# Kernel optimization log

Hardware: AMD Instinct MI355X
Metric: run time of the kernel (lower is better)

## Reference

```python
import jax, jax.numpy as jnp
import numpy as np

N, E, G = 2048, 4096, 128      # nodes, edges, graphs
H, IN, ED = 128, 11, 4         # hidden, input node feat, edge feat
BN_EPS = 1e-5


def setup_inputs() -> dict:
    key = jax.random.key(0)
    ks = iter(jax.random.split(key, 40))
    r = lambda shape, s=0.1: jax.random.normal(next(ks), shape, jnp.float32) * s
    inp = dict(
        x=r((N, IN), 1.0),
        edge_attr=jax.random.uniform(next(ks), (E, ED), jnp.float32),
        edge_index=jax.random.randint(next(ks), (2, E), 0, N).astype(jnp.int32),
        batch=jnp.sort(jax.random.randint(next(ks), (N,), 0, G)).astype(jnp.int32),
        # layer 0 (in=11 -> out=128)
        w1_0=r((ED, H)), b1_0=jnp.zeros(H), w2_0=r((H, IN * H), 0.02), b2_0=jnp.zeros(IN * H),
        root_0=r((IN, H)), bias_0=jnp.zeros(H),
        bn_g0=jnp.ones(H), bn_b0=jnp.zeros(H), bn_m0=r((H,), 0.1),
        bn_v0=jax.random.uniform(next(ks), (H,), jnp.float32, 0.5, 1.5),
        # layers 1..4 stacked (in=out=128)
        w1_s=r((4, ED, H)), b1_s=jnp.zeros((4, H)), w2_s=r((4, H, H * H), 0.02), b2_s=jnp.zeros((4, H * H)),
        root_s=r((4, H, H)), bias_s=jnp.zeros((4, H)),
        bn_gs=jnp.ones((4, H)), bn_bs=jnp.zeros((4, H)), bn_ms=r((4, H), 0.1),
        bn_vs=jax.random.uniform(next(ks), (4, H), jnp.float32, 0.5, 1.5),
        # readout MLP
        lin1_w=r((H, H // 2)), lin1_b=jnp.zeros(H // 2),
        lin2_w=r((H // 2, 1)), lin2_b=jnp.zeros(1),
    )
    return inp


def _nnconv(x, src, dst, edge_attr, w1, b1, w2, b2, root, bias):
    in_c = x.shape[-1]
    h = jax.nn.relu(edge_attr @ w1 + b1)                 # [E, H]
    w_e = (h @ w2 + b2).reshape(-1, in_c, H)             # [E, in, H] per-edge weight
    msg = jnp.einsum('ei,eio->eo', x[src], w_e)          # gather + per-edge matvec
    s = jax.ops.segment_sum(msg, dst, num_segments=N)
    cnt = jax.ops.segment_sum(jnp.ones(dst.shape, x.dtype), dst, num_segments=N)
    aggr = s / jnp.maximum(cnt, 1.0)[:, None]            # scatter-mean
    return aggr + x @ root + bias


def _bn_eval(x, g, b, m, v):
    return (x - m) * jax.lax.rsqrt(v + BN_EPS) * g + b


def reference(x, edge_attr, w1_0, b1_0, w2_0, b2_0, root_0, bias_0,
              bn_g0, bn_b0, bn_m0, bn_v0,
              w1_s, b1_s, w2_s, b2_s, root_s, bias_s,
              bn_gs, bn_bs, bn_ms, bn_vs,
              lin1_w, lin1_b, lin2_w, lin2_b,
              edge_index, batch):
    src, dst = edge_index[0], edge_index[1]
    # layer 0
    h = jax.nn.relu(_bn_eval(
        _nnconv(x, src, dst, edge_attr, w1_0, b1_0, w2_0, b2_0, root_0, bias_0),
        bn_g0, bn_b0, bn_m0, bn_v0))
    # layers 1..4 with residual (dims match)
    for l in range(4):
        h_new = jax.nn.relu(_bn_eval(
            _nnconv(h, src, dst, edge_attr, w1_s[l], b1_s[l], w2_s[l], b2_s[l], root_s[l], bias_s[l]),
            bn_gs[l], bn_bs[l], bn_ms[l], bn_vs[l]))
        h = h + h_new
    # global mean pool over graphs
    gs = jax.ops.segment_sum(h, batch, num_segments=G)
    gc = jax.ops.segment_sum(jnp.ones((N,), h.dtype), batch, num_segments=G)
    g = gs / jnp.maximum(gc, 1.0)[:, None]
    # readout (dropout is identity in eval mode)
    g = jax.nn.relu(g @ lin1_w + lin1_b)
    return g @ lin2_w + lin2_b
```

## Files before the change

### kernel.cpp

```cpp
#include <hip/hip_runtime.h>
#include <cstdint>
#include <cstddef>

#define NN 2048
#define NE 4096
#define NG 128
#define HD 128
#define SKM 16
#define SK0 5
#define NCH 64
#define CHE 64

typedef __attribute__((ext_vector_type(8))) _Float16 f16x8;
typedef __attribute__((ext_vector_type(4))) float f32x4;

#define GLOAD_LDS16(gptr, lptr)                                                          \
  __builtin_amdgcn_global_load_lds((const __attribute__((address_space(1))) unsigned int*)(gptr), \
                                   (__attribute__((address_space(3))) unsigned int*)(lptr), 16, 0, 0)

__global__ __launch_bounds__(256) void k_prep(
    const float* __restrict__ ea,
    const float* __restrict__ w1_0, const float* __restrict__ b1_0,
    const float* __restrict__ w1_s, const float* __restrict__ b1_s,
    const float* __restrict__ x,
    const float* __restrict__ w2_0, const float* __restrict__ b2_0,
    const float* __restrict__ w2s, const float* __restrict__ b2s,
    const int* __restrict__ dst, int* __restrict__ hist,
    _Float16* __restrict__ hb, _Float16* __restrict__ x16,
    _Float16* __restrict__ w2T0, _Float16* __restrict__ w2T) {
  __shared__ float sld[64][65];
  const int bid = blockIdx.x, t = threadIdx.x;

  if (bid < 10240) {
    int idx = bid * 256 + t;
    int c = idx & (HD - 1);
    int e = (idx >> 7) & (NE - 1);
    int l = idx >> 19;
    const float* w1 = (l == 0) ? w1_0 : (w1_s + (size_t)(l - 1) * 4 * HD);
    const float* b1 = (l == 0) ? b1_0 : (b1_s + (size_t)(l - 1) * HD);
    float4 a = *(const float4*)(ea + (size_t)e * 4);
    float v = b1[c] + a.x * w1[c] + a.y * w1[HD + c] + a.z * w1[2 * HD + c] + a.w * w1[3 * HD + c];
    hb[idx] = (_Float16)fmaxf(v, 0.f);
  } else if (bid < 10368) {
    int idx = (bid - 10240) * 256 + t;
    int n = idx >> 4, i = idx & 15;
    x16[idx] = (_Float16)(i < 11 ? x[(size_t)n * 11 + i] : 0.f);
  } else if (bid < 10496) {
    int o = bid - 10368;
    for (int kap = t; kap < 2080; kap += 256) {
      int k = kap >> 4, i = kap & 15;
      float v = 0.f;
      if (i < 11) {
        if (k < 128) v = w2_0[(size_t)k * 1408 + i * 128 + o];
        else if (k == 128) v = b2_0[i * 128 + o];
      }
      w2T0[(size_t)o * 2080 + kap] = (_Float16)v;
    }
  } else if (bid < 12560) {
    int idx2 = bid - 10496;
    int l = idx2 / 516;
    int rem = idx2 - l * 516;
    int ob = rem / 258;
    int kb = rem - ob * 258;
    const float* w2 = w2s + (size_t)l * 16384 * 128;
    const float* b2 = b2s + (size_t)l * 128 * 128;
    _Float16* outp = w2T + (size_t)l * 128 * 16512;
    int k0 = kb * 64, o0 = ob * 64;
    int r = t >> 4, c4 = (t & 15) * 4;
#pragma unroll
    for (int it = 0; it < 4; ++it) {
      int kk = k0 + r + it * 16;
      const float* srcp = (kk < 16384) ? (w2 + (size_t)kk * 128 + o0 + c4)
                                       : (b2 + (size_t)(kk - 16384) * 128 + o0 + c4);
      *(float4*)&sld[r + it * 16][c4] = *(const float4*)srcp;
    }
    __syncthreads();
    int rr = t >> 3, c8 = (t & 7) * 8;
#pragma unroll
    for (int it = 0; it < 2; ++it) {
      int ol = rr + it * 32;
      _Float16 pk[8];
#pragma unroll
      for (int j = 0; j < 8; ++j) pk[j] = (_Float16)sld[c8 + j][ol];
      *(f16x8*)(outp + (size_t)(o0 + ol) * 16512 + k0 + c8) = *(const f16x8*)pk;
    }
  } else {
    int e = (bid - 12560) * 256 + t;
    if (e < NE) atomicAdd(&hist[(e >> 6) * NN + dst[e]], 1);
  }
}

__global__ __launch_bounds__(1024) void k_scan2(const int* __restrict__ hist,
                                                int* __restrict__ rowptr,
                                                int* __restrict__ chunkoff,
                                                const int* __restrict__ batch,
                                                int* __restrict__ gstart) {
  __shared__ int s[NN];
  int t = threadIdx.x;
  int c0 = 0, c1 = 0;
  for (int c = 0; c < NCH; ++c) { c0 += hist[c * NN + t]; c1 += hist[c * NN + t + 1024]; }
  s[t] = c0; s[t + 1024] = c1;
  __syncthreads();
  for (int d = 1; d < NN; d <<= 1) {
    int a0 = s[t], a1 = s[t + 1024];
    int v0 = (t >= d) ? s[t - d] : 0;
    int v1 = (t + 1024 >= d) ? s[t + 1024 - d] : 0;
    __syncthreads();
    s[t] = a0 + v0; s[t + 1024] = a1 + v1;
    __syncthreads();
  }
  rowptr[t + 1] = s[t]; rowptr[t + 1025] = s[t + 1024];
  if (t == 0) rowptr[0] = 0;
  int run0 = s[t] - c0, run1 = s[t + 1024] - c1;
  for (int c = 0; c < NCH; ++c) {
    chunkoff[c * NN + t] = run0;        run0 += hist[c * NN + t];
    chunkoff[c * NN + t + 1024] = run1; run1 += hist[c * NN + t + 1024];
  }
  if (t <= NG) {
    int lo = 0, hi = NN;
    while (lo < hi) { int mid = (lo + hi) >> 1; if (batch[mid] < t) lo = mid + 1; else hi = mid; }
    gstart[t] = lo;
  }
}

__global__ __launch_bounds__(64) void k_fill2(const int* __restrict__ dst,
                                              const int* __restrict__ chunkoff,
                                              int* __restrict__ elist) {
  __shared__ int sd[CHE];
  int c = blockIdx.x, t = threadIdx.x;
  int e = c * CHE + t;
  int dv = dst[e];
  sd[t] = dv;
  __syncthreads();
  int lrank = 0;
  for (int j = 0; j < t; ++j) lrank += (sd[j] == dv) ? 1 : 0;
  elist[chunkoff[c * NN + dv] + lrank] = e;
}

__global__ __launch_bounds__(256, 2) void k_mma0(
    const _Float16* __restrict__ xh,
    const _Float16* __restrict__ hb,
    const _Float16* __restrict__ w2T,
    const int* __restrict__ src,
    _Float16* __restrict__ msgp) {
  constexpr int KT = 2080;
  __shared__ _Float16 Bs[2][4096];
  __shared__ _Float16 hTl[26][128];

  const int tid = threadIdx.x;
  const int e0 = blockIdx.x * 128;
  const int w = tid >> 6, l = tid & 63, l16 = l & 15, g = l >> 4;

  const int k0 = blockIdx.y * 13, nk = 13;
  const int kb = k0 * 2;

  int nd[8];
#pragma unroll
  for (int mt = 0; mt < 8; ++mt) nd[mt] = src[e0 + mt * 16 + l16];

  for (int idx = tid; idx < 26 * 128; idx += 256) {
    int kk = idx >> 7, m = idx & 127;
    int k = kb + kk;
    _Float16 v;
    if (k < 128) v = hb[(size_t)(e0 + m) * 128 + k];
    else v = (k == 128) ? (_Float16)1.0f : (_Float16)0.0f;
    hTl[kk][m] = v;
  }

  f16x8 xr[8];
#pragma unroll
  for (int mt = 0; mt < 8; ++mt)
    xr[mt] = *(const f16x8*)(xh + (size_t)nd[mt] * 16 + (g & 1) * 8);

  auto stageB = [&](int buf, int c) {
    const int kap0 = c * 32;
#pragma unroll
    for (int j2 = 0; j2 < 2; ++j2) {
      int ntg = w * 2 + j2;
      const _Float16* gp = w2T + (size_t)(ntg * 16 + l16) * KT + kap0 + g * 8;
      GLOAD_LDS16(gp, &Bs[buf][(w * 128 + j2 * 64) * 8]);
    }
  };

  stageB(0, k0);
  __syncthreads();

  f32x4 acc[8][2];
#pragma unroll
  for (int mt = 0; mt < 8; ++mt)
#pragma unroll
    for (int jj = 0; jj < 2; ++jj) acc[mt][jj] = (f32x4){0.f, 0.f, 0.f, 0.f};

  int buf = 0;
  for (int j = 0; j < nk; ++j) {
    if (j + 1 < nk) {
      stageB(buf ^ 1, k0 + j + 1);
      asm volatile("s_waitcnt vmcnt(2)" ::: "memory");
    } else {
      asm volatile("s_waitcnt vmcnt(0)" ::: "memory");
    }
    __builtin_amdgcn_sched_barrier(0);

    f16x8 bv0 = *(const f16x8*)&Bs[buf][(size_t)(w * 2 + 0) * 512 + l * 8];
    f16x8 bv1 = *(const f16x8*)&Bs[buf][(size_t)(w * 2 + 1) * 512 + l * 8];
#pragma unroll
    for (int mt = 0; mt < 8; ++mt) {
      _Float16 hh = hTl[2 * j + (g >> 1)][mt * 16 + l16];
      f16x8 hv = {hh, hh, hh, hh, hh, hh, hh, hh};
      f16x8 av = xr[mt] * hv;
      acc[mt][0] = __builtin_amdgcn_mfma_f32_16x16x32_f16(av, bv0, acc[mt][0], 0, 0, 0);
      acc[mt][1] = __builtin_amdgcn_mfma_f32_16x16x32_f16(av, bv1, acc[mt][1], 0, 0, 0);
    }
    buf ^= 1;
    __syncthreads();
  }

  _Float16* mp = msgp + ((size_t)blockIdx.y * NE + e0) * 128;
#pragma unroll
  for (int mt = 0; mt < 8; ++mt)
#pragma unroll
    for (int jj = 0; jj < 2; ++jj)
#pragma unroll
      for (int r = 0; r < 4; ++r) {
        int row = mt * 16 + 4 * g + r;
        mp[(size_t)row * 128 + w * 32 + jj * 16 + l16] = (_Float16)acc[mt][jj][r];
      }
}

__global__ __launch_bounds__(256, 2) void k_mma4(
    const _Float16* __restrict__ xh,
    const _Float16* __restrict__ hb,
    const _Float16* __restrict__ w2T,
    const int* __restrict__ src,
    _Float16* __restrict__ msgp) {
  constexpr int KT = 16512;
  __shared__ __align__(16) _Float16 Bs[2][4096];

  const int tid = threadIdx.x;
  const int w = tid >> 6, l = tid & 63, l16 = l & 15, g = l >> 4;
  const int e0 = blockIdx.x * 128;
  const int sk = blockIdx.y;
  const int k0 = sk * 8;
  const bool haveBias = (sk == 15);

  int nd[8];
#pragma unroll
  for (int mt = 0; mt < 8; ++mt) nd[mt] = src[e0 + mt * 16 + l16];

  f16x8 hv[8];
#pragma unroll
  for (int mt = 0; mt < 8; ++mt)
    hv[mt] = *(const f16x8*)(hb + (size_t)(e0 + mt * 16 + l16) * 128 + k0);

  auto stageB = [&](int buf, int kap0) {
#pragma unroll
    for (int j2 = 0; j2 < 2; ++j2) {
      const _Float16* gp = w2T + (size_t)((w * 2 + j2) * 16 + l16) * KT + kap0 + g * 8;
      GLOAD_LDS16(gp, &Bs[buf][(w * 2 + j2) * 512]);
    }
  };

  f32x4 acc[8][2];
#pragma unroll
  for (int mt = 0; mt < 8; ++mt) {
    acc[mt][0] = (f32x4){0.f, 0.f, 0.f, 0.f};
    acc[mt][1] = (f32x4){0.f, 0.f, 0.f, 0.f};
  }

  int buf = 0;
  stageB(0, k0 * 128);

#define CONSUME(AV_EXPR)                                                              \
  {                                                                                   \
    f16x8 bv0 = *(const f16x8*)&Bs[buf][(w * 2 + 0) * 512 + l * 8];                   \
    f16x8 bv1 = *(const f16x8*)&Bs[buf][(w * 2 + 1) * 512 + l * 8];                   \
    _Pragma("unroll")                                                                 \
    for (int mt = 0; mt < 8; ++mt) {                                                  \
      f16x8 av = (AV_EXPR);                                                           \
      acc[mt][0] = __builtin_amdgcn_mfma_f32_16x16x32_f16(av, bv0, acc[mt][0], 0, 0, 0); \
      acc[mt][1] = __builtin_amdgcn_mfma_f32_16x16x32_f16(av, bv1, acc[mt][1], 0, 0, 0); \
    }                                                                                 \
    buf ^= 1;                                                                         \
  }

#pragma unroll
  for (int win = 0; win < 4; ++win) {
    f16x8 xw[8];
#pragma unroll
    for (int mt = 0; mt < 8; ++mt)
      xw[mt] = *(const f16x8*)(xh + (size_t)nd[mt] * 128 + win * 32 + g * 8);

#pragma unroll
    for (int jk = 0; jk < 8; ++jk) {
      if (jk < 7) {
        stageB(buf ^ 1, (k0 + jk + 1) * 128 + win * 32);
        asm volatile("s_waitcnt vmcnt(2)" ::: "memory");
      } else if (haveBias) {
        stageB(buf ^ 1, 16384 + win * 32);
        asm volatile("s_waitcnt vmcnt(2)" ::: "memory");
      } else if (win < 3) {
        stageB(buf ^ 1, k0 * 128 + (win + 1) * 32);
        asm volatile("s_waitcnt vmcnt(2)" ::: "memory");
      } else {
        asm volatile("s_waitcnt vmcnt(0)" ::: "memory");
      }
      __builtin_amdgcn_sched_barrier(0);
      _Float16 hh;
      CONSUME(({ hh = hv[mt][jk];
                 f16x8 hs = {hh, hh, hh, hh, hh, hh, hh, hh};
                 xw[mt] * hs; }));
    }
    if (haveBias) {
      if (win < 3) {
        stageB(buf ^ 1, k0 * 128 + (win + 1) * 32);
        asm volatile("s_waitcnt vmcnt(2)" ::: "memory");
      } else {
        asm volatile("s_waitcnt vmcnt(0)" ::: "memory");
      }
      __builtin_amdgcn_sched_barrier(0);
      CONSUME((xw[mt]));
    }
  }
#undef CONSUME

  _Float16* mp = msgp + ((size_t)sk * NE + e0) * 128;
#pragma unroll
  for (int mt = 0; mt < 8; ++mt)
#pragma unroll
    for (int jj = 0; jj < 2; ++jj)
#pragma unroll
      for (int r = 0; r < 4; ++r) {
        int row = mt * 16 + 4 * g + r;
        mp[(size_t)row * 128 + w * 32 + jj * 16 + l16] = (_Float16)acc[mt][jj][r];
      }
}

template <int NSK>
__global__ __launch_bounds__(256) void k_msum(const _Float16* __restrict__ msgp,
                                              float* __restrict__ msgf) {
  int idx = blockIdx.x * 256 + threadIdx.x;
  const _Float16* p = msgp + (size_t)idx * 8;
  float s0 = 0.f, s1 = 0.f, s2 = 0.f, s3 = 0.f, s4 = 0.f, s5 = 0.f, s6 = 0.f, s7 = 0.f;
#pragma unroll
  for (int k = 0; k < NSK; ++k) {
    f16x8 v = *(const f16x8*)(p + (size_t)k * NE * HD);
    s0 += (float)v[0]; s1 += (float)v[1]; s2 += (float)v[2]; s3 += (float)v[3];
    s4 += (float)v[4]; s5 += (float)v[5]; s6 += (float)v[6]; s7 += (float)v[7];
  }
  float4* o = (float4*)(msgf + (size_t)idx * 8);
  o[0] = (float4){s0, s1, s2, s3};
  o[1] = (float4){s4, s5, s6, s7};
}

template <int INR>
__global__ void k_au(const float* __restrict__ msgf, const int* __restrict__ rowptr,
                     const int* __restrict__ elist, const float* __restrict__ xin,
                     const float* __restrict__ root, const float* __restrict__ bias,
                     const float* __restrict__ bg, const float* __restrict__ bb,
                     const float* __restrict__ bm, const float* __restrict__ bv,
                     const float* __restrict__ h_prev, float* __restrict__ h_out,
                     _Float16* __restrict__ h_out_h) {
  int n = blockIdx.x, t = threadIdx.x;
  __shared__ float xr[INR];
  if (t < INR) xr[t] = xin[(size_t)n * INR + t];
  int beg = rowptr[n], end = rowptr[n + 1];
  float v = 0.f;
  for (int j = beg; j < end; ++j) v += msgf[(size_t)elist[j] * HD + t];
  v /= fmaxf((float)(end - beg), 1.f);
  __syncthreads();
  float acc = v + bias[t];
  if constexpr (INR == 128) {
    float a0 = 0.f, a1 = 0.f, a2 = 0.f, a3 = 0.f;
#pragma unroll 4
    for (int k = 0; k < 128; k += 4) {
      a0 += xr[k + 0] * root[(size_t)(k + 0) * HD + t];
      a1 += xr[k + 1] * root[(size_t)(k + 1) * HD + t];
      a2 += xr[k + 2] * root[(size_t)(k + 2) * HD + t];
      a3 += xr[k + 3] * root[(size_t)(k + 3) * HD + t];
    }
    acc += (a0 + a1) + (a2 + a3);
  } else {
#pragma unroll
    for (int k = 0; k < INR; ++k) acc += xr[k] * root[(size_t)k * HD + t];
  }
  float bn = (acc - bm[t]) * rsqrtf(bv[t] + 1e-5f) * bg[t] + bb[t];
  float r = fmaxf(bn, 0.f);
  float val = h_prev ? (h_prev[(size_t)n * HD + t] + r) : r;
  h_out[(size_t)n * HD + t] = val;
  h_out_h[(size_t)n * HD + t] = (_Float16)val;
}

__global__ void k_poolread(const float* __restrict__ h, const int* __restrict__ gstart,
                           const float* __restrict__ w1, const float* __restrict__ b1,
                           const float* __restrict__ w2, const float* __restrict__ b2,
                           float* __restrict__ out) {
  int g = blockIdx.x, t = threadIdx.x;
  __shared__ float row[HD];
  int beg = gstart[g], end = gstart[g + 1];
  float v = 0.f;
  for (int n = beg; n < end; ++n) v += h[(size_t)n * HD + t];
  row[t] = v / fmaxf((float)(end - beg), 1.f);
  __syncthreads();
  if (t < 64) {
    float acc = b1[t];
#pragma unroll 8
    for (int k = 0; k < HD; ++k) acc += row[k] * w1[(size_t)k * 64 + t];
    float vv = fmaxf(acc, 0.f) * w2[t];
#pragma unroll
    for (int off = 32; off > 0; off >>= 1) vv += __shfl_down(vv, off);
    if (t == 0) out[g] = vv + b2[0];
  }
}

extern "C" void kernel_launch(void* const* d_in, const int* in_sizes, int n_in,
                              void* d_out, int out_size, void* d_ws, size_t ws_size,
                              hipStream_t stream) {
  const float* x      = (const float*)d_in[0];
  const float* ea     = (const float*)d_in[1];
  const int*   eidx   = (const int*)d_in[2];
  const int*   batch  = (const int*)d_in[3];
  const float* w1_0   = (const float*)d_in[4];
  const float* b1_0   = (const float*)d_in[5];
  const float* w2_0   = (const float*)d_in[6];
  const float* b2_0   = (const float*)d_in[7];
  const float* root_0 = (const float*)d_in[8];
  const float* bias_0 = (const float*)d_in[9];
  const float* bn_g0  = (const float*)d_in[10];
  const float* bn_b0  = (const float*)d_in[11];
  const float* bn_m0  = (const float*)d_in[12];
  const float* bn_v0  = (const float*)d_in[13];
  const float* w1_s   = (const float*)d_in[14];
  const float* b1_s   = (const float*)d_in[15];
  const float* w2_s   = (const float*)d_in[16];
  const float* b2_s   = (const float*)d_in[17];
  const float* root_s = (const float*)d_in[18];
  const float* bias_s = (const float*)d_in[19];
  const float* bn_gs  = (const float*)d_in[20];
  const float* bn_bs  = (const float*)d_in[21];
  const float* bn_ms  = (const float*)d_in[22];
  const float* bn_vs  = (const float*)d_in[23];
  const float* lin1_w = (const float*)d_in[24];
  const float* lin1_b = (const float*)d_in[25];
  const float* lin2_w = (const float*)d_in[26];
  const float* lin2_b = (const float*)d_in[27];
  float* out = (float*)d_out;

  char* wsb = (char*)d_ws;
  size_t off = 0;
  auto alloc = [&](size_t bytes) { void* p = wsb + off; off = (off + bytes + 255) & ~(size_t)255; return p; };
  int*      rowptr   = (int*)alloc((NN + 4) * 4);
  int*      elist    = (int*)alloc(NE * 4);
  int*      gstart   = (int*)alloc((NG + 4) * 4);
  int*      hist     = (int*)alloc((size_t)NCH * NN * 4);
  int*      chunkoff = (int*)alloc((size_t)NCH * NN * 4);
  _Float16* hbf      = (_Float16*)alloc((size_t)5 * NE * HD * 2);
  _Float16* x16      = (_Float16*)alloc((size_t)NN * 16 * 2);
  _Float16* w2T0     = (_Float16*)alloc((size_t)128 * 2080 * 2);
  _Float16* w2T      = (_Float16*)alloc((size_t)4 * 128 * 16512 * 2);
  float*    hnA      = (float*)alloc((size_t)NN * HD * 4);
  float*    hnB      = (float*)alloc((size_t)NN * HD * 4);
  _Float16* hnAh     = (_Float16*)alloc((size_t)NN * HD * 2);
  _Float16* hnBh     = (_Float16*)alloc((size_t)NN * HD * 2);
  _Float16* msgp     = (_Float16*)alloc((size_t)SKM * NE * HD * 2);
  float*    msgf     = (float*)alloc((size_t)NE * HD * 4);

  const int* src = eidx;
  const int* dstp = eidx + NE;

  hipMemsetAsync(hist, 0, (size_t)NCH * NN * 4, stream);
  k_prep<<<dim3(12576), 256, 0, stream>>>(ea, w1_0, b1_0, w1_s, b1_s, x,
                                          w2_0, b2_0, w2_s, b2_s,
                                          dstp, hist, hbf, x16, w2T0, w2T);
  k_scan2<<<1, 1024, 0, stream>>>(hist, rowptr, chunkoff, batch, gstart);
  k_fill2<<<dim3(NCH), 64, 0, stream>>>(dstp, chunkoff, elist);

  k_mma0<<<dim3(NE / 128, SK0), 256, 0, stream>>>(x16, hbf, w2T0, src, msgp);
  k_msum<SK0><<<dim3(256), 256, 0, stream>>>(msgp, msgf);
  k_au<11><<<NN, HD, 0, stream>>>(msgf, rowptr, elist, x, root_0, bias_0,
                                  bn_g0, bn_b0, bn_m0, bn_v0, nullptr, hnA, hnAh);

  float* cur = hnA;  _Float16* curh = hnAh;
  float* nxt = hnB;  _Float16* nxth = hnBh;
  for (int l = 1; l <= 4; ++l) {
    const _Float16* w2Tl = w2T + (size_t)(l - 1) * 128 * 16512;
    k_mma4<<<dim3(NE / 128, SKM), 256, 0, stream>>>(curh, hbf + (size_t)l * NE * HD,
                                                    w2Tl, src, msgp);
    k_msum<SKM><<<dim3(256), 256, 0, stream>>>(msgp, msgf);
    k_au<128><<<NN, HD, 0, stream>>>(msgf, rowptr, elist, cur,
                                     root_s + (size_t)(l - 1) * HD * HD,
                                     bias_s + (size_t)(l - 1) * HD,
                                     bn_gs + (size_t)(l - 1) * HD, bn_bs + (size_t)(l - 1) * HD,
                                     bn_ms + (size_t)(l - 1) * HD, bn_vs + (size_t)(l - 1) * HD,
                                     cur, nxt, nxth);
    float* tf = cur; cur = nxt; nxt = tf;
    _Float16* th = curh; curh = nxth; nxth = th;
  }

  k_poolread<<<NG, HD, 0, stream>>>(cur, gstart, lin1_w, lin1_b, lin2_w, lin2_b, out);
}
```

Baseline: 246.6 us.

## Deepen k_mma4 weight prefetch to four LDS buffers and flatten grid

The B-operand staging in the per-layer MFMA kernel moves from double buffering to a four-deep ring with three stages in flight, and the bias pass moves to the end using its own staging. The launch grid is flattened so split-K slices of the same edge block run adjacently. The intent is to hide more global-to-LDS load latency and improve cache reuse of gathered node rows. This doubles LDS usage per block, which may affect occupancy.

New measurement: 277.7 us. 1.13x slower.

```diff
diff --git a/kernel.cpp b/kernel.cpp
--- a/kernel.cpp
+++ b/kernel.cpp
@@ -17,6 +17,8 @@
 #define GLOAD_LDS16(gptr, lptr)                                                          \
   __builtin_amdgcn_global_load_lds((const __attribute__((address_space(1))) unsigned int*)(gptr), \
                                    (__attribute__((address_space(3))) unsigned int*)(lptr), 16, 0, 0)
+
+#define VMW(n) asm volatile("s_waitcnt vmcnt(" #n ")" ::: "memory")
 
 __global__ __launch_bounds__(256) void k_prep(
     const float* __restrict__ ea,
@@ -234,12 +236,13 @@
     const int* __restrict__ src,
     _Float16* __restrict__ msgp) {
   constexpr int KT = 16512;
-  __shared__ __align__(16) _Float16 Bs[2][4096];
+  __shared__ __align__(16) _Float16 Bs[4][4096];
 
   const int tid = threadIdx.x;
   const int w = tid >> 6, l = tid & 63, l16 = l & 15, g = l >> 4;
-  const int e0 = blockIdx.x * 128;
-  const int sk = blockIdx.y;
+  const int bid = blockIdx.x;
+  const int eb = bid >> 4, sk = bid & 15;
+  const int e0 = eb * 128;
   const int k0 = sk * 8;
   const bool haveBias = (sk == 15);
 
@@ -259,6 +262,7 @@
       GLOAD_LDS16(gp, &Bs[buf][(w * 2 + j2) * 512]);
     }
   };
+  auto kapOf = [&](int s) { return (k0 + (s & 7)) * 128 + (s >> 3) * 32; };
 
   f32x4 acc[8][2];
 #pragma unroll
@@ -267,20 +271,21 @@
     acc[mt][1] = (f32x4){0.f, 0.f, 0.f, 0.f};
   }
 
-  int buf = 0;
-  stageB(0, k0 * 128);
-
-#define CONSUME(AV_EXPR)                                                              \
-  {                                                                                   \
-    f16x8 bv0 = *(const f16x8*)&Bs[buf][(w * 2 + 0) * 512 + l * 8];                   \
-    f16x8 bv1 = *(const f16x8*)&Bs[buf][(w * 2 + 1) * 512 + l * 8];                   \
-    _Pragma("unroll")                                                                 \
-    for (int mt = 0; mt < 8; ++mt) {                                                  \
-      f16x8 av = (AV_EXPR);                                                           \
+  stageB(0, kapOf(0));
+  stageB(1, kapOf(1));
+  stageB(2, kapOf(2));
+
+#define CONSUME_S(S, AV_EXPR)                                                          \
+  {                                                                                    \
+    const int buf_ = (S) & 3;                                                          \
+    f16x8 bv0 = *(const f16x8*)&Bs[buf_][(w * 2 + 0) * 512 + l * 8];                   \
+    f16x8 bv1 = *(const f16x8*)&Bs[buf_][(w * 2 + 1) * 512 + l * 8];                   \
+    _Pragma("unroll")                                                                  \
+    for (int mt = 0; mt < 8; ++mt) {                                                   \
+      f16x8 av = (AV_EXPR);                                                            \
       acc[mt][0] = __builtin_amdgcn_mfma_f32_16x16x32_f16(av, bv0, acc[mt][0], 0, 0, 0); \
       acc[mt][1] = __builtin_amdgcn_mfma_f32_16x16x32_f16(av, bv1, acc[mt][1], 0, 0, 0); \
-    }                                                                                 \
-    buf ^= 1;                                                                         \
+    }                                                                                  \
   }
 
 #pragma unroll
@@ -292,36 +297,41 @@
 
 #pragma unroll
     for (int jk = 0; jk < 8; ++jk) {
-      if (jk < 7) {
-        stageB(buf ^ 1, (k0 + jk + 1) * 128 + win * 32);
-        asm volatile("s_waitcnt vmcnt(2)" ::: "memory");
+      const int s = win * 8 + jk;
+      const int nxt = s + 3;
+      if (nxt < 32) {
+        stageB(nxt & 3, kapOf(nxt));
+        VMW(6);
       } else if (haveBias) {
-        stageB(buf ^ 1, 16384 + win * 32);
-        asm volatile("s_waitcnt vmcnt(2)" ::: "memory");
-      } else if (win < 3) {
-        stageB(buf ^ 1, k0 * 128 + (win + 1) * 32);
-        asm volatile("s_waitcnt vmcnt(2)" ::: "memory");
+        stageB(nxt & 3, 16384 + (nxt - 32) * 32);
+        VMW(6);
       } else {
-        asm volatile("s_waitcnt vmcnt(0)" ::: "memory");
+        if (nxt == 32) { VMW(4); }
+        else if (nxt == 33) { VMW(2); }
+        else { VMW(0); }
       }
       __builtin_amdgcn_sched_barrier(0);
       _Float16 hh;
-      CONSUME(({ hh = hv[mt][jk];
-                 f16x8 hs = {hh, hh, hh, hh, hh, hh, hh, hh};
-                 xw[mt] * hs; }));
-    }
-    if (haveBias) {
-      if (win < 3) {
-        stageB(buf ^ 1, k0 * 128 + (win + 1) * 32);
-        asm volatile("s_waitcnt vmcnt(2)" ::: "memory");
-      } else {
-        asm volatile("s_waitcnt vmcnt(0)" ::: "memory");
-      }
+      CONSUME_S(s, ({ hh = hv[mt][jk];
+                      f16x8 hs = {hh, hh, hh, hh, hh, hh, hh, hh};
+                      xw[mt] * hs; }));
+    }
+  }
+
+  if (haveBias) {
+    stageB(3, 16384 + 3 * 32);
+#pragma unroll
+    for (int b = 0; b < 4; ++b) {
+      f16x8 xb[8];
+#pragma unroll
+      for (int mt = 0; mt < 8; ++mt)
+        xb[mt] = *(const f16x8*)(xh + (size_t)nd[mt] * 128 + b * 32 + g * 8);
+      VMW(0);
       __builtin_amdgcn_sched_barrier(0);
-      CONSUME((xw[mt]));
-    }
-  }
-#undef CONSUME
+      CONSUME_S(32 + b, (xb[mt]));
+    }
+  }
+#undef CONSUME_S
 
   _Float16* mp = msgp + ((size_t)sk * NE + e0) * 128;
 #pragma unroll
@@ -483,8 +493,8 @@
   float* nxt = hnB;  _Float16* nxth = hnBh;
   for (int l = 1; l <= 4; ++l) {
     const _Float16* w2Tl = w2T + (size_t)(l - 1) * 128 * 16512;
-    k_mma4<<<dim3(NE / 128, SKM), 256, 0, stream>>>(curh, hbf + (size_t)l * NE * HD,
-                                                    w2Tl, src, msgp);
+    k_mma4<<<dim3((NE / 128) * SKM), 256, 0, stream>>>(curh, hbf + (size_t)l * NE * HD,
+                                                       w2Tl, src, msgp);
     k_msum<SKM><<<dim3(256), 256, 0, stream>>>(msgp, msgf);
     k_au<128><<<NN, HD, 0, stream>>>(msgf, rowptr, elist, cur,
                                      root_s + (size_t)(l - 1) * HD * HD,
```
